# Kernel optimization log

Hardware: AMD Instinct MI355X
Metric: run time of the kernel (lower is better)

The kernel has to match this reference:

```python
import jax, jax.numpy as jnp
import numpy as np

N_NODES = 500_000
N_EDGES = 16_000_000


def setup_inputs() -> dict:
    key = jax.random.key(0)
    k1, k2, k3, k4 = jax.random.split(key, 4)
    x = jax.random.normal(k1, (N_NODES, 1), dtype=jnp.float32)
    edge_index = jax.random.randint(k2, (2, N_EDGES), 0, N_NODES, dtype=jnp.int64)
    W1 = jax.random.normal(k3, (1, 8), dtype=jnp.float32) * (1.0 / np.sqrt(1))
    b1 = jnp.zeros((8,), dtype=jnp.float32)
    W2 = jax.random.normal(k4, (8, 2), dtype=jnp.float32) * (1.0 / np.sqrt(8))
    b2 = jnp.zeros((2,), dtype=jnp.float32)
    return {"x": x, "edge_index": edge_index, "W1": W1, "b1": b1, "W2": W2, "b2": b2}


def _gcn_conv(x, src, dst, norm, W, b):
    # PyG GCNConv: h = X W; out_i = sum_{(j->i)} norm_ji * h_j + b
    h = x @ W                         # [N, out]
    msg = h[src] * norm[:, None]      # [E', out] gather + scale
    out = jax.ops.segment_sum(msg, dst, num_segments=N_NODES)  # scatter-add
    return out + b


def reference(x, edge_index, W1, b1, W2, b2):
    # add self-loops (PyG default add_self_loops=True)
    loop = jnp.arange(N_NODES, dtype=edge_index.dtype)
    src = jnp.concatenate([edge_index[0], loop])
    dst = jnp.concatenate([edge_index[1], loop])
    # symmetric normalization: deg^{-1/2}[src] * deg^{-1/2}[dst]
    deg = jax.ops.segment_sum(jnp.ones_like(dst, dtype=x.dtype), dst, num_segments=N_NODES)
    dis = jnp.where(deg > 0, jax.lax.rsqrt(deg), 0.0)
    norm = dis[src] * dis[dst]        # [E']
    h = jax.nn.relu(_gcn_conv(x, src, dst, norm, W1, b1))
    return _gcn_conv(h, src, dst, norm, W2, b2)
```

## Files before the change

kernel.cpp:

```cpp
#include <hip/hip_runtime.h>
#include <hip/hip_fp16.h>

#define N_NODES 500000
typedef unsigned int u32;
typedef unsigned short u16;

#define NPB    512
#define NBUCK  ((N_NODES + NPB - 1) / NPB)
#define CAP    20480
#define CH     8192
#define EPT    8
#define STB    1024
#define LTB    512
#define SRC19  0x7FFFFu

typedef unsigned int v4u __attribute__((ext_vector_type(4)));
__device__ inline int  nt1i(const int* p) { return __builtin_nontemporal_load(p); }
__device__ inline u32  nt1u(const u32* p) { return __builtin_nontemporal_load(p); }
__device__ inline v4u  nt4u(const u32* p) { return __builtin_nontemporal_load((const v4u*)p); }

__device__ inline float ldh(const u16* p) {
    __half h = *(const __half*)p;
    return __half2float(h);
}
__device__ inline u16 sth(float v) {
    __half h = __float2half(v);
    return *(u16*)&h;
}
__device__ inline u32 pack2h(float a, float b) {
    union { __half2 h; u32 u; } cvt;
    cvt.h = __floats2half2_rn(a, b);
    return cvt.u;
}
__device__ inline float2 unpack2h(u32 w) {
    union { u32 u; __half2 h; } cvt;
    cvt.u = w;
    return __half22float2(cvt.h);
}

__global__ __launch_bounds__(STB) void k_scatter_fused(
        const int* __restrict__ src, const int* __restrict__ dst, int E,
        u32* __restrict__ cur_g, u32* __restrict__ rec) {
    __shared__ u32 srec[CH];
    __shared__ u16 sbk[CH];
    __shared__ u32 hist[NBUCK];
    __shared__ u32 sc[1024];
    __shared__ u32 scn_ex[NBUCK];
    __shared__ u32 cur2[NBUCK];
    __shared__ u32 gbase[NBUCK];
    int tid = threadIdx.x, bid = blockIdx.x;
    for (int b = tid; b < NBUCK; b += STB) hist[b] = 0;
    __syncthreads();
    int e0 = bid * CH, e1 = min(E, e0 + CH), n = e1 - e0;
    u32 dv[EPT], sv[EPT];
#pragma unroll
    for (int k = 0; k < EPT; ++k) {
        int e = e0 + (k << 10) + tid;
        if (e < e1) {
            dv[k] = (u32)nt1i(dst + e);
            sv[k] = (u32)nt1i(src + e);
            atomicAdd(&hist[dv[k] >> 9], 1u);
        }
    }
    __syncthreads();
    sc[tid] = (tid < NBUCK) ? hist[tid] : 0u;
    __syncthreads();
    for (int off = 1; off < 1024; off <<= 1) {
        u32 t = (tid >= off) ? sc[tid - off] : 0u;
        __syncthreads();
        sc[tid] += t;
        __syncthreads();
    }
    if (tid < NBUCK) {
        u32 ex = sc[tid] - hist[tid];
        scn_ex[tid] = ex;
        cur2[tid] = ex;
        gbase[tid] = hist[tid] ? atomicAdd(&cur_g[tid], hist[tid]) : 0u;
    }
    __syncthreads();
#pragma unroll
    for (int k = 0; k < EPT; ++k) {
        int e = e0 + (k << 10) + tid;
        if (e < e1) {
            u32 b = dv[k] >> 9;
            u32 p = atomicAdd(&cur2[b], 1u);
            srec[p] = ((dv[k] & (NPB - 1u)) << 19) | sv[k];
            sbk[p] = (u16)b;
        }
    }
    __syncthreads();
    for (int p = tid; p < n; p += STB) {
        u32 b = sbk[p];
        u32 slot = gbase[b] + ((u32)p - scn_ex[b]);
        rec[(size_t)b * CAP + slot] = srec[p];
    }
}

__global__ __launch_bounds__(LTB) void k_deg_dis(
        const u32* __restrict__ rec, const u32* __restrict__ cnt_g,
        const float* __restrict__ x,
        float* __restrict__ dis, u16* __restrict__ m1h) {
    __shared__ u32 cnt[NPB];
    int tid = threadIdx.x, bid = blockIdx.x;
    for (int l = tid; l < NPB; l += LTB) cnt[l] = 0;
    __syncthreads();
    const u32* r0 = rec + (size_t)bid * CAP;
    u32 n = cnt_g[bid];
    u32 nv = n >> 2;
    for (u32 i = tid; i < nv; i += LTB) {
        v4u r = nt4u(r0 + ((size_t)i << 2));
        atomicAdd(&cnt[r.x >> 19], 1u);
        atomicAdd(&cnt[r.y >> 19], 1u);
        atomicAdd(&cnt[r.z >> 19], 1u);
        atomicAdd(&cnt[r.w >> 19], 1u);
    }
    for (u32 e = (nv << 2) + tid; e < n; e += LTB)
        atomicAdd(&cnt[nt1u(r0 + e) >> 19], 1u);
    __syncthreads();
    int node0 = bid << 9;
    int nn = min(NPB, N_NODES - node0);
    for (int l = tid; l < nn; l += LTB) {
        int node = node0 + l;
        float r = rsqrtf((float)(cnt[l] + 1u));
        dis[node] = r;
        m1h[node] = sth(r * x[node]);
    }
}

__global__ __launch_bounds__(LTB) void k_layer1(
        const u32* __restrict__ rec, const u32* __restrict__ cnt_g,
        const float* __restrict__ dis, const u16* __restrict__ m1h,
        const float* __restrict__ W1, const float* __restrict__ b1,
        const float* __restrict__ W2, const float* __restrict__ b2,
        u32* __restrict__ h2mh, float2* __restrict__ out) {
    __shared__ float acc[NPB];
    int tid = threadIdx.x, bid = blockIdx.x;
    for (int l = tid; l < NPB; l += LTB) acc[l] = 0.f;
    __syncthreads();
    const u32* r0 = rec + (size_t)bid * CAP;
    u32 n = cnt_g[bid];
    u32 nv = n >> 2;
    for (u32 i = tid; i < nv; i += LTB) {
        v4u r = nt4u(r0 + ((size_t)i << 2));
        float v0 = ldh(m1h + (r.x & SRC19));
        float v1 = ldh(m1h + (r.y & SRC19));
        float v2 = ldh(m1h + (r.z & SRC19));
        float v3 = ldh(m1h + (r.w & SRC19));
        atomicAdd(&acc[r.x >> 19], v0);
        atomicAdd(&acc[r.y >> 19], v1);
        atomicAdd(&acc[r.z >> 19], v2);
        atomicAdd(&acc[r.w >> 19], v3);
    }
    for (u32 e = (nv << 2) + tid; e < n; e += LTB) {
        u32 r = nt1u(r0 + e);
        atomicAdd(&acc[r >> 19], ldh(m1h + (r & SRC19)));
    }
    __syncthreads();
    int node0 = bid << 9;
    int nn = min(NPB, N_NODES - node0);
    for (int l = tid; l < nn; l += LTB) {
        int node = node0 + l;
        float d = dis[node];
        float s = d * (acc[l] + ldh(m1h + node));
        float a0 = 0.f, a1 = 0.f;
#pragma unroll
        for (int k = 0; k < 8; ++k) {
            float h = fmaxf(W1[k] * s + b1[k], 0.f);
            a0 += h * W2[2 * k + 0];
            a1 += h * W2[2 * k + 1];
        }
        h2mh[node] = pack2h(d * a0, d * a1);
        out[node] = make_float2(b2[0] + d * d * a0, b2[1] + d * d * a1);
    }
}

__global__ __launch_bounds__(LTB) void k_layer2(
        const u32* __restrict__ rec, const u32* __restrict__ cnt_g,
        const float* __restrict__ dis, const u32* __restrict__ h2mh,
        float2* __restrict__ out) {
    __shared__ float ax[NPB];
    __shared__ float ay[NPB];
    int tid = threadIdx.x, bid = blockIdx.x;
    for (int l = tid; l < NPB; l += LTB) { ax[l] = 0.f; ay[l] = 0.f; }
    __syncthreads();
    const u32* r0 = rec + (size_t)bid * CAP;
    u32 n = cnt_g[bid];
    u32 nv = n >> 2;
    for (u32 i = tid; i < nv; i += LTB) {
        v4u r = nt4u(r0 + ((size_t)i << 2));
        float2 v0 = unpack2h(h2mh[r.x & SRC19]);
        float2 v1 = unpack2h(h2mh[r.y & SRC19]);
        float2 v2 = unpack2h(h2mh[r.z & SRC19]);
        float2 v3 = unpack2h(h2mh[r.w & SRC19]);
        atomicAdd(&ax[r.x >> 19], v0.x);
        atomicAdd(&ay[r.x >> 19], v0.y);
        atomicAdd(&ax[r.y >> 19], v1.x);
        atomicAdd(&ay[r.y >> 19], v1.y);
        atomicAdd(&ax[r.z >> 19], v2.x);
        atomicAdd(&ay[r.z >> 19], v2.y);
        atomicAdd(&ax[r.w >> 19], v3.x);
        atomicAdd(&ay[r.w >> 19], v3.y);
    }
    for (u32 e = (nv << 2) + tid; e < n; e += LTB) {
        u32 r = nt1u(r0 + e);
        float2 v = unpack2h(h2mh[r & SRC19]);
        atomicAdd(&ax[r >> 19], v.x);
        atomicAdd(&ay[r >> 19], v.y);
    }
    __syncthreads();
    int node0 = bid << 9;
    int nn = min(NPB, N_NODES - node0);
    for (int l = tid; l < nn; l += LTB) {
        int node = node0 + l;
        float d = dis[node];
        float2 o = out[node];
        out[node] = make_float2(o.x + d * ax[l], o.y + d * ay[l]);
    }
}

__global__ void f_count_deg(const int* __restrict__ dst, int E,
                            u32* __restrict__ deg) {
    int i = blockIdx.x * blockDim.x + threadIdx.x;
    int stride = gridDim.x * blockDim.x;
    for (int e = i; e < E; e += stride) atomicAdd(&deg[dst[e]], 1u);
}
__global__ void f_dis_sinit(const u32* __restrict__ deg, const float* __restrict__ x,
                            float* __restrict__ dis, float* __restrict__ s, int N) {
    int i = blockIdx.x * blockDim.x + threadIdx.x;
    if (i < N) {
        float r = rsqrtf((float)(deg[i] + 1u));
        dis[i] = r;
        s[i] = r * r * x[i];
    }
}
__global__ void f_agg1(const int* __restrict__ src, const int* __restrict__ dst,
                       int E, const float* __restrict__ dis,
                       const float* __restrict__ x, float* __restrict__ s) {
    int i = blockIdx.x * blockDim.x + threadIdx.x;
    int stride = gridDim.x * blockDim.x;
    for (int e = i; e < E; e += stride) {
        int sj = src[e], dj = dst[e];
        atomicAdd(&s[dj], dis[sj] * dis[dj] * x[sj]);
    }
}
__global__ void f_node2(const float* __restrict__ s, const float* __restrict__ dis,
                        const float* __restrict__ W1, const float* __restrict__ b1,
                        const float* __restrict__ W2, const float* __restrict__ b2,
                        float2* __restrict__ h2, float2* __restrict__ out, int N) {
    int i = blockIdx.x * blockDim.x + threadIdx.x;
    if (i >= N) return;
    float si = s[i];
    float a0 = 0.f, a1 = 0.f;
#pragma unroll
    for (int k = 0; k < 8; ++k) {
        float hk = fmaxf(W1[k] * si + b1[k], 0.f);
        a0 += hk * W2[2 * k + 0];
        a1 += hk * W2[2 * k + 1];
    }
    h2[i] = make_float2(a0, a1);
    float r2 = dis[i] * dis[i];
    out[i] = make_float2(b2[0] + r2 * a0, b2[1] + r2 * a1);
}
__global__ void f_agg2(const int* __restrict__ src, const int* __restrict__ dst,
                       int E, const float* __restrict__ dis,
                       const float2* __restrict__ h2, float* __restrict__ out) {
    int i = blockIdx.x * blockDim.x + threadIdx.x;
    int stride = gridDim.x * blockDim.x;
    for (int e = i; e < E; e += stride) {
        int sj = src[e], dj = dst[e];
        float nm = dis[sj] * dis[dj];
        float2 v = h2[sj];
        atomicAdd(&out[2 * dj + 0], nm * v.x);
        atomicAdd(&out[2 * dj + 1], nm * v.y);
    }
}

extern "C" void kernel_launch(void* const* d_in, const int* in_sizes, int n_in,
                              void* d_out, int out_size, void* d_ws, size_t ws_size,
                              hipStream_t stream) {
    const float* x  = (const float*)d_in[0];
    const int*   ei = (const int*)d_in[1];
    const float* W1 = (const float*)d_in[2];
    const float* b1 = (const float*)d_in[3];
    const float* W2 = (const float*)d_in[4];
    const float* b2 = (const float*)d_in[5];

    const int N = N_NODES;
    const int E = in_sizes[1] / 2;
    const int* src = ei;
    const int* dst = ei + E;
    float* out = (float*)d_out;
    char* ws = (char*)d_ws;

    size_t off = 0;
    auto take = [&](size_t bytes) { size_t o = off; off = (off + bytes + 255) & ~(size_t)255; return o; };
    size_t off_cur  = take(NBUCK * 4);
    size_t off_dis  = take((size_t)N * 4);
    size_t off_m1h  = take((size_t)N * 2);
    size_t off_h2mh = take((size_t)N * 4);
    size_t off_rec  = take((size_t)NBUCK * CAP * 4 + 16);
    size_t need     = off;

    if (ws_size >= need) {
        u32* cur_g  = (u32*)(ws + off_cur);
        float* dis  = (float*)(ws + off_dis);
        u16* m1h    = (u16*)(ws + off_m1h);
        u32* h2mh   = (u32*)(ws + off_h2mh);
        u32* rec    = (u32*)(ws + off_rec);

        hipMemsetAsync(cur_g, 0, NBUCK * 4, stream);
        const int nchunks = (E + CH - 1) / CH;
        k_scatter_fused<<<nchunks, STB, 0, stream>>>(src, dst, E, cur_g, rec);
        k_deg_dis      <<<NBUCK,   LTB, 0, stream>>>(rec, cur_g, x, dis, m1h);
        k_layer1       <<<NBUCK,   LTB, 0, stream>>>(rec, cur_g, dis, m1h,
                                                     W1, b1, W2, b2,
                                                     h2mh, (float2*)out);
        k_layer2       <<<NBUCK,   LTB, 0, stream>>>(rec, cur_g, dis, h2mh,
                                                     (float2*)out);
        return;
    }

    u32* deg    = (u32*)(ws);
    float* dis  = (float*)(ws + (size_t)N * 4);
    float* s    = (float*)(ws + (size_t)N * 8);
    float2* h2  = (float2*)(ws + (size_t)N * 12);
    hipMemsetAsync(deg, 0, (size_t)N * 4, stream);
    int nodeBlocks = (N + 255) / 256;
    int edgeBlocks = (E + 255) / 256;
    f_count_deg<<<edgeBlocks, 256, 0, stream>>>(dst, E, deg);
    f_dis_sinit<<<nodeBlocks, 256, 0, stream>>>(deg, x, dis, s, N);
    f_agg1     <<<edgeBlocks, 256, 0, stream>>>(src, dst, E, dis, x, s);
    f_node2    <<<nodeBlocks, 256, 0, stream>>>(s, dis, W1, b1, W2, b2, h2,
                                                (float2*)out, N);
    f_agg2     <<<edgeBlocks, 256, 0, stream>>>(src, dst, E, dis, h2, out);
}
```

Measured before the change: 514.9 us.

## Pack layer-2 accumulators into biased fixed-point u64 LDS atomics

Layer 2 now converts each gathered half2 message to two biased 32-bit fixed-point values packed into one u64 and accumulates them with a single 64-bit LDS atomic, replacing two float LDS atomics per edge. The bias is subtracted afterwards using a per-node degree stored in a new u16 array written by the degree kernel. Layer-1 gathers of m1h also switch to nontemporal loads. This halves the shared-memory atomic count in layer 2 but adds fixed-point quantization and relies on the bias and degree to keep the low word from carrying into the high word.

```diff
diff --git a/kernel.cpp b/kernel.cpp
--- a/kernel.cpp
+++ b/kernel.cpp
@@ -4,6 +4,7 @@
 #define N_NODES 500000
 typedef unsigned int u32;
 typedef unsigned short u16;
+typedef unsigned long long u64;
 
 #define NPB    512
 #define NBUCK  ((N_NODES + NPB - 1) / NPB)
@@ -14,6 +15,10 @@
 #define LTB    512
 #define SRC19  0x7FFFFu
 
+#define FXS    524288.0f
+#define FXSI   1.9073486328e-6f
+#define FXB    16777216u
+
 typedef unsigned int v4u __attribute__((ext_vector_type(4)));
 __device__ inline int  nt1i(const int* p) { return __builtin_nontemporal_load(p); }
 __device__ inline u32  nt1u(const u32* p) { return __builtin_nontemporal_load(p); }
@@ -23,6 +28,11 @@
     __half h = *(const __half*)p;
     return __half2float(h);
 }
+__device__ inline float ldhnt(const u16* p) {
+    u16 raw = __builtin_nontemporal_load(p);
+    __half h = *(__half*)&raw;
+    return __half2float(h);
+}
 __device__ inline u16 sth(float v) {
     __half h = __float2half(v);
     return *(u16*)&h;
@@ -36,6 +46,11 @@
     union { u32 u; __half2 h; } cvt;
     cvt.u = w;
     return __half22float2(cvt.h);
+}
+__device__ inline u64 packfx(float2 v) {
+    u32 ex = (u32)__float2int_rn(v.x * FXS) + FXB;
+    u32 ey = (u32)__float2int_rn(v.y * FXS) + FXB;
+    return ((u64)ey << 32) | (u64)ex;
 }
 
 __global__ __launch_bounds__(STB) void k_scatter_fused(
@@ -99,7 +114,8 @@
 __global__ __launch_bounds__(LTB) void k_deg_dis(
         const u32* __restrict__ rec, const u32* __restrict__ cnt_g,
         const float* __restrict__ x,
-        float* __restrict__ dis, u16* __restrict__ m1h) {
+        float* __restrict__ dis, u16* __restrict__ m1h,
+        u16* __restrict__ deg16) {
     __shared__ u32 cnt[NPB];
     int tid = threadIdx.x, bid = blockIdx.x;
     for (int l = tid; l < NPB; l += LTB) cnt[l] = 0;
@@ -121,9 +137,11 @@
     int nn = min(NPB, N_NODES - node0);
     for (int l = tid; l < nn; l += LTB) {
         int node = node0 + l;
-        float r = rsqrtf((float)(cnt[l] + 1u));
+        u32 c = cnt[l];
+        float r = rsqrtf((float)(c + 1u));
         dis[node] = r;
         m1h[node] = sth(r * x[node]);
+        deg16[node] = (u16)c;
     }
 }
 
@@ -142,10 +160,10 @@
     u32 nv = n >> 2;
     for (u32 i = tid; i < nv; i += LTB) {
         v4u r = nt4u(r0 + ((size_t)i << 2));
-        float v0 = ldh(m1h + (r.x & SRC19));
-        float v1 = ldh(m1h + (r.y & SRC19));
-        float v2 = ldh(m1h + (r.z & SRC19));
-        float v3 = ldh(m1h + (r.w & SRC19));
+        float v0 = ldhnt(m1h + (r.x & SRC19));
+        float v1 = ldhnt(m1h + (r.y & SRC19));
+        float v2 = ldhnt(m1h + (r.z & SRC19));
+        float v3 = ldhnt(m1h + (r.w & SRC19));
         atomicAdd(&acc[r.x >> 19], v0);
         atomicAdd(&acc[r.y >> 19], v1);
         atomicAdd(&acc[r.z >> 19], v2);
@@ -153,7 +171,7 @@
     }
     for (u32 e = (nv << 2) + tid; e < n; e += LTB) {
         u32 r = nt1u(r0 + e);
-        atomicAdd(&acc[r >> 19], ldh(m1h + (r & SRC19)));
+        atomicAdd(&acc[r >> 19], ldhnt(m1h + (r & SRC19)));
     }
     __syncthreads();
     int node0 = bid << 9;
@@ -177,11 +195,10 @@
 __global__ __launch_bounds__(LTB) void k_layer2(
         const u32* __restrict__ rec, const u32* __restrict__ cnt_g,
         const float* __restrict__ dis, const u32* __restrict__ h2mh,
-        float2* __restrict__ out) {
-    __shared__ float ax[NPB];
-    __shared__ float ay[NPB];
+        const u16* __restrict__ deg16, float2* __restrict__ out) {
+    __shared__ u64 sacc[NPB];
     int tid = threadIdx.x, bid = blockIdx.x;
-    for (int l = tid; l < NPB; l += LTB) { ax[l] = 0.f; ay[l] = 0.f; }
+    for (int l = tid; l < NPB; l += LTB) sacc[l] = 0ull;
     __syncthreads();
     const u32* r0 = rec + (size_t)bid * CAP;
     u32 n = cnt_g[bid];
@@ -192,29 +209,28 @@
         float2 v1 = unpack2h(h2mh[r.y & SRC19]);
         float2 v2 = unpack2h(h2mh[r.z & SRC19]);
         float2 v3 = unpack2h(h2mh[r.w & SRC19]);
-        atomicAdd(&ax[r.x >> 19], v0.x);
-        atomicAdd(&ay[r.x >> 19], v0.y);
-        atomicAdd(&ax[r.y >> 19], v1.x);
-        atomicAdd(&ay[r.y >> 19], v1.y);
-        atomicAdd(&ax[r.z >> 19], v2.x);
-        atomicAdd(&ay[r.z >> 19], v2.y);
-        atomicAdd(&ax[r.w >> 19], v3.x);
-        atomicAdd(&ay[r.w >> 19], v3.y);
+        atomicAdd(&sacc[r.x >> 19], packfx(v0));
+        atomicAdd(&sacc[r.y >> 19], packfx(v1));
+        atomicAdd(&sacc[r.z >> 19], packfx(v2));
+        atomicAdd(&sacc[r.w >> 19], packfx(v3));
     }
     for (u32 e = (nv << 2) + tid; e < n; e += LTB) {
         u32 r = nt1u(r0 + e);
         float2 v = unpack2h(h2mh[r & SRC19]);
-        atomicAdd(&ax[r >> 19], v.x);
-        atomicAdd(&ay[r >> 19], v.y);
+        atomicAdd(&sacc[r >> 19], packfx(v));
     }
     __syncthreads();
     int node0 = bid << 9;
     int nn = min(NPB, N_NODES - node0);
     for (int l = tid; l < nn; l += LTB) {
         int node = node0 + l;
+        u64 a = sacc[l];
+        u32 dgB = (u32)deg16[node] * FXB;
+        float sx = (float)(int)((u32)a - dgB) * FXSI;
+        float sy = (float)(int)((u32)(a >> 32) - dgB) * FXSI;
         float d = dis[node];
         float2 o = out[node];
-        out[node] = make_float2(o.x + d * ax[l], o.y + d * ay[l]);
+        out[node] = make_float2(o.x + d * sx, o.y + d * sy);
     }
 }
 
@@ -298,6 +314,7 @@
     size_t off_dis  = take((size_t)N * 4);
     size_t off_m1h  = take((size_t)N * 2);
     size_t off_h2mh = take((size_t)N * 4);
+    size_t off_dg   = take((size_t)N * 2);
     size_t off_rec  = take((size_t)NBUCK * CAP * 4 + 16);
     size_t need     = off;
 
@@ -306,17 +323,19 @@
         float* dis  = (float*)(ws + off_dis);
         u16* m1h    = (u16*)(ws + off_m1h);
         u32* h2mh   = (u32*)(ws + off_h2mh);
+        u16* deg16  = (u16*)(ws + off_dg);
         u32* rec    = (u32*)(ws + off_rec);
 
         hipMemsetAsync(cur_g, 0, NBUCK * 4, stream);
         const int nchunks = (E + CH - 1) / CH;
         k_scatter_fused<<<nchunks, STB, 0, stream>>>(src, dst, E, cur_g, rec);
-        k_deg_dis      <<<NBUCK,   LTB, 0, stream>>>(rec, cur_g, x, dis, m1h);
+        k_deg_dis      <<<NBUCK,   LTB, 0, stream>>>(rec, cur_g, x, dis, m1h,
+                                                     deg16);
         k_layer1       <<<NBUCK,   LTB, 0, stream>>>(rec, cur_g, dis, m1h,
                                                      W1, b1, W2, b2,
                                                      h2mh, (float2*)out);
         k_layer2       <<<NBUCK,   LTB, 0, stream>>>(rec, cur_g, dis, h2mh,
-                                                     (float2*)out);
+                                                     deg16, (float2*)out);
         return;
     }
 
```

Result: faster. 466.4 us (-9.4%).
